# Optimization experiments

Measured on AMD Instinct MI355X. Metric: run time of the kernel, lower is better.

## Reference

```python
import jax, jax.numpy as jnp
import numpy as np

N = 100000
E = 1000000
P = 1000000
HID = 128
ROLE_VOCAB = 8
ROLE_DIM = 16
IDX_VOCAB = 1024
IDX_DIM = 8
FEAT = 14
IN_DIM = FEAT + IDX_DIM + ROLE_DIM  # 38


def setup_inputs() -> dict:
    key = jax.random.key(0)
    ks = jax.random.split(key, 20)
    s = 0.02
    return {
        "block_features": jax.random.normal(ks[0], (N, FEAT), jnp.float32),
        "role_ids": jax.random.randint(ks[1], (N,), 0, ROLE_VOCAB),
        "b2b_src": jax.random.randint(ks[2], (E,), 0, N),
        "b2b_dst": jax.random.randint(ks[3], (E,), 0, N),
        "b2b_w": jax.random.uniform(ks[4], (E,), jnp.float32),
        "p2b_block": jax.random.randint(ks[5], (P,), 0, N),
        "p2b_w": jax.random.uniform(ks[6], (P,), jnp.float32),
        "role_emb": jax.random.normal(ks[7], (ROLE_VOCAB, ROLE_DIM), jnp.float32),
        "idx_emb": jax.random.normal(ks[8], (IDX_VOCAB, IDX_DIM), jnp.float32),
        "W1": jax.random.normal(ks[9], (IN_DIM, HID), jnp.float32) * s,
        "b1": jnp.zeros((HID,), jnp.float32),
        "W2": jax.random.normal(ks[10], (HID, HID), jnp.float32) * s,
        "b2": jnp.zeros((HID,), jnp.float32),
        "M1": jax.random.normal(ks[11], (HID, HID), jnp.float32) * s,
        "mb1": jnp.zeros((HID,), jnp.float32),
        "M2": jax.random.normal(ks[12], (HID, HID), jnp.float32) * s,
        "mb2": jnp.zeros((HID,), jnp.float32),
        "ln_g": jnp.ones((HID,), jnp.float32),
        "ln_b": jnp.zeros((HID,), jnp.float32),
    }


def _layernorm(x, g, b, eps=1e-5):
    mu = jnp.mean(x, axis=-1, keepdims=True)
    var = jnp.mean(jnp.square(x - mu), axis=-1, keepdims=True)
    return (x - mu) * jax.lax.rsqrt(var + eps) * g + b


def reference(block_features, role_ids, b2b_src, b2b_dst, b2b_w, p2b_block, p2b_w,
              role_emb, idx_emb, W1, b1, W2, b2, M1, mb1, M2, mb2, ln_g, ln_b):
    n = block_features.shape[0]
    # embeddings + input MLP
    re = role_emb[role_ids]                                  # [N, 16]
    ie = idx_emb[jnp.arange(n) % IDX_VOCAB]                  # [N, 8]
    x = jnp.concatenate([block_features, re, ie], axis=-1)   # [N, 38]
    h = jax.nn.relu(x @ W1 + b1)
    emb = jax.nn.relu(h @ W2 + b2)                           # [N, HID]
    # b2b: symmetric weighted scatter-add of neighbor embeddings
    agg = jnp.zeros_like(emb)
    agg = agg.at[b2b_src].add(emb[b2b_dst] * b2b_w[:, None])
    agg = agg.at[b2b_dst].add(emb[b2b_src] * b2b_w[:, None])
    # p2b: agg[j] += emb[j] * w  ==  emb * (sum of pin weights per block)
    pw = jnp.zeros((n,), emb.dtype).at[p2b_block].add(p2b_w)
    agg = agg + emb * pw[:, None]
    # message MLP + residual + LayerNorm
    m = jax.nn.relu(agg @ M1 + mb1) @ M2 + mb2
    block_embeddings = _layernorm(emb + m, ln_g, ln_b)
    graph_embedding = jnp.mean(block_embeddings, axis=0)
    return block_embeddings, graph_embedding
```

## Files before the change

kernel.cpp:

```cpp
#include <hip/hip_runtime.h>

#define FEAT 14
#define ROLE_DIM 16
#define IDX_DIM 8
#define IN_DIM 38
#define HID 128
#define IDX_VOCAB 1024
#define BINN 128
#define NBINS_MAX 800
#define TILE_E 2048
#define CAPT 16
#define SCAP 64
#define SORT_CAP 4096

typedef __attribute__((ext_vector_type(8))) short short8;
typedef __attribute__((ext_vector_type(4))) float f32x4;
typedef __attribute__((ext_vector_type(2))) float f32x2;

__device__ __forceinline__ ushort f2bf(float f) {
    uint u = __float_as_uint(f);
    return (ushort)((u + 0x7FFFu + ((u >> 16) & 1u)) >> 16);
}
__device__ __forceinline__ float bf2f(ushort h) {
    return __uint_as_float((uint)h << 16);
}
__device__ __forceinline__ uchar f2fp8(float f) {
    return (uchar)(__builtin_amdgcn_cvt_pk_fp8_f32(f, f, 0, false) & 0xff);
}

__global__ void k_prep(const float* __restrict__ W1, const float* __restrict__ W2,
                       const float* __restrict__ M1, const float* __restrict__ M2,
                       ushort* __restrict__ W1t, ushort* __restrict__ W2t,
                       ushort* __restrict__ M1t, ushort* __restrict__ M2t)
{
    int t = blockIdx.x * 256 + threadIdx.x;
    if (t < 8192) {
        int c = t >> 6, k = t & 63;
        W1t[t] = (k < IN_DIM) ? f2bf(W1[k * HID + c]) : (ushort)0;
    } else if (t < 24576) {
        int u = t - 8192; int c = u >> 7, k = u & 127;
        W2t[u] = f2bf(W2[k * HID + c]);
    } else if (t < 40960) {
        int u = t - 24576; int c = u >> 7, k = u & 127;
        M1t[u] = f2bf(M1[k * HID + c]);
    } else if (t < 57344) {
        int u = t - 40960; int c = u >> 7, k = u & 127;
        M2t[u] = f2bf(M2[k * HID + c]);
    }
}

#define LDSA 32768

__global__ __launch_bounds__(256) void k_embed_mlp(
    const float* __restrict__ feat, const int* __restrict__ role_ids,
    const float* __restrict__ role_emb, const float* __restrict__ idx_emb,
    const ushort* __restrict__ W1t, const float* __restrict__ b1,
    const ushort* __restrict__ W2t, const float* __restrict__ b2,
    ushort* __restrict__ embh, uchar* __restrict__ embf8, int N)
{
    __shared__ char lds[49152];
    const int tid = threadIdx.x;
    const int w = tid >> 6, l = tid & 63;
    const int li = l & 15, hi = l >> 4;
    const int base = blockIdx.x * 64;

    for (int c = 0; c < 4; ++c) {
        int idx = c * 256 + tid;
        int col = idx >> 3, ch = idx & 7;
        uint4 v = *(const uint4*)(W1t + col * 64 + ch * 8);
        *(uint4*)(lds + col * 256 + ((ch * 16) ^ ((col & 7) << 4))) = v;
    }
    {
        int row = tid >> 2, kq = (tid & 3) * 16;
        int gr = base + row; if (gr >= N) gr = N - 1;
        int rid = role_ids[gr];
        float xv[16];
        #pragma unroll
        for (int j = 0; j < 16; ++j) {
            int k = kq + j;
            float v = 0.0f;
            if (k < FEAT)                 v = feat[gr * FEAT + k];
            else if (k < FEAT + ROLE_DIM) v = role_emb[rid * ROLE_DIM + (k - FEAT)];
            else if (k < IN_DIM)          v = idx_emb[(gr & (IDX_VOCAB - 1)) * IDX_DIM + (k - FEAT - ROLE_DIM)];
            xv[j] = v;
        }
        uint p[8];
        #pragma unroll
        for (int j = 0; j < 8; ++j)
            p[j] = (uint)f2bf(xv[2 * j]) | ((uint)f2bf(xv[2 * j + 1]) << 16);
        char* db = lds + LDSA + row * 256;
        int sw = (row & 7) << 4;
        *(uint4*)(db + ((kq * 2) ^ sw))      = make_uint4(p[0], p[1], p[2], p[3]);
        *(uint4*)(db + ((kq * 2 + 16) ^ sw)) = make_uint4(p[4], p[5], p[6], p[7]);
    }
    __syncthreads();

    f32x4 C[8];
    #pragma unroll
    for (int ct = 0; ct < 8; ++ct) C[ct] = (f32x4){0.f, 0.f, 0.f, 0.f};
    {
        const int arow = w * 16 + li;
        const int asw = (arow & 7) << 4;
        #pragma unroll
        for (int ks = 0; ks < 2; ++ks) {
            short8 a = *(short8*)(lds + LDSA + arow * 256 + ((ks * 64 + hi * 16) ^ asw));
            #pragma unroll
            for (int ct = 0; ct < 8; ++ct) {
                int bcol = ct * 16 + li;
                short8 b = *(short8*)(lds + bcol * 256 + ((ks * 64 + hi * 16) ^ ((bcol & 7) << 4)));
                C[ct] = __builtin_amdgcn_mfma_f32_16x16x32_bf16(a, b, C[ct], 0, 0, 0);
            }
        }
    }
    __syncthreads();

    #pragma unroll
    for (int ct = 0; ct < 8; ++ct) {
        int col = ct * 16 + li;
        float bv = b1[col];
        #pragma unroll
        for (int r = 0; r < 4; ++r) {
            int hrow = w * 16 + hi * 4 + r;
            float h = fmaxf(C[ct][r] + bv, 0.0f);
            *(ushort*)(lds + LDSA + hrow * 256 + ((col * 2) ^ ((hrow & 7) << 4))) = f2bf(h);
        }
    }
    for (int c = 0; c < 8; ++c) {
        int idx = c * 256 + tid;
        int col = idx >> 4, ch = idx & 15;
        uint4 v = *(const uint4*)(W2t + col * 128 + ch * 8);
        *(uint4*)(lds + col * 256 + ((ch * 16) ^ ((col & 7) << 4))) = v;
    }
    __syncthreads();

    f32x4 C2[8];
    #pragma unroll
    for (int ct = 0; ct < 8; ++ct) C2[ct] = (f32x4){0.f, 0.f, 0.f, 0.f};
    {
        const int arow = w * 16 + li;
        const int asw = (arow & 7) << 4;
        #pragma unroll
        for (int ks = 0; ks < 4; ++ks) {
            short8 a = *(short8*)(lds + LDSA + arow * 256 + ((ks * 64 + hi * 16) ^ asw));
            #pragma unroll
            for (int ct = 0; ct < 8; ++ct) {
                int bcol = ct * 16 + li;
                short8 b = *(short8*)(lds + bcol * 256 + ((ks * 64 + hi * 16) ^ ((bcol & 7) << 4)));
                C2[ct] = __builtin_amdgcn_mfma_f32_16x16x32_bf16(a, b, C2[ct], 0, 0, 0);
            }
        }
    }

    #pragma unroll
    for (int ct = 0; ct < 8; ++ct) {
        int col = ct * 16 + li;
        float bv = b2[col];
        #pragma unroll
        for (int r = 0; r < 4; ++r) {
            int gr = base + w * 16 + hi * 4 + r;
            if (gr < N) {
                float o = fmaxf(C2[ct][r] + bv, 0.0f);
                embh[(size_t)gr * 128 + col] = f2bf(o);
                embf8[(size_t)gr * 128 + col] = f2fp8(o);
            }
        }
    }
}

__global__ __launch_bounds__(1024) void k_binp(
    const int* __restrict__ src, const int* __restrict__ dst,
    const float* __restrict__ w, uint* __restrict__ staged,
    int* __restrict__ cnt,
    const int* __restrict__ pb, const float* __restrict__ pv,
    float* __restrict__ pw,
    int E, int P, int nbins, int chunk, int chunkP)
{
    __shared__ uint buf[NBINS_MAX * CAPT];
    __shared__ int curT[NBINS_MAX];
    __shared__ int segCur[NBINS_MAX];
    const int tid = threadIdx.x;
    const int blk = blockIdx.x;
    for (int i = tid; i < nbins; i += 1024) { curT[i] = 0; segCur[i] = 0; }
    __syncthreads();

    const int lo = blk * chunk;
    const int hiE = (lo + chunk) < E ? (lo + chunk) : E;
    for (int t0 = lo; t0 < hiE; t0 += TILE_E) {
        int t1 = t0 + TILE_E; if (t1 > hiE) t1 = hiE;
        for (int i = t0 + tid; i < t1; i += 1024) {
            int s = src[i], d = dst[i];
            uint q = (uint)(w[i] * 255.0f + 0.5f);
            int bs = s >> 7;
            uint es = ((uint)(s & 127) << 25) | ((uint)d << 8) | q;
            int ps = atomicAdd(&curT[bs], 1);
            if (ps < CAPT) buf[bs * CAPT + ps] = es;
            else { int gp = segCur[bs] + ps;
                   if (gp < SCAP) staged[((size_t)bs * 256 + blk) * SCAP + gp] = es; }
            int bd = d >> 7;
            uint ed = ((uint)(d & 127) << 25) | ((uint)s << 8) | q;
            int pd = atomicAdd(&curT[bd], 1);
            if (pd < CAPT) buf[bd * CAPT + pd] = ed;
            else { int gp = segCur[bd] + pd;
                   if (gp < SCAP) staged[((size_t)bd * 256 + blk) * SCAP + gp] = ed; }
        }
        __syncthreads();
        for (int b = tid; b < nbins; b += 1024) {
            int tot = curT[b];
            int base = segCur[b];
            int k = tot < CAPT ? tot : CAPT;
            if (base + k > SCAP) { k = SCAP - base; if (k < 0) k = 0; }
            uint* dp = staged + ((size_t)b * 256 + blk) * SCAP + base;
            for (int i = 0; i < k; ++i) dp[i] = buf[b * CAPT + i];
            segCur[b] = base + tot;
            curT[b] = 0;
        }
        __syncthreads();
    }
    for (int i = tid; i < nbins; i += 1024)
        cnt[blk * nbins + i] = segCur[i] < SCAP ? segCur[i] : SCAP;

    int loP = blk * chunkP;
    int hiP = loP + chunkP; if (hiP > P) hiP = P;
    for (int i = loP + tid; i < hiP; i += 1024)
        atomicAdd(&pw[pb[i]], pv[i]);
}

__global__ __launch_bounds__(256) void k_agg(
    const uint* __restrict__ staged, const int* __restrict__ cnt,
    const ushort* __restrict__ embh, const uchar* __restrict__ embf8,
    const float* __restrict__ pw,
    ushort* __restrict__ aggh, int N, int nbins)
{
    __shared__ int hist[BINN];
    __shared__ int startL[BINN];
    __shared__ int curL[BINN];
    __shared__ int sc[BINN];
    __shared__ uint sorted[SORT_CAP];

    const int tid = threadIdx.x;
    const int b = blockIdx.x;
    const int baseNode = b << 7;

    if (tid < BINN) hist[tid] = 0;
    __syncthreads();

    const int c = cnt[tid * nbins + b];
    const uint* sp = staged + ((size_t)b * 256 + tid) * SCAP;
    for (int k = 0; k < c; ++k)
        atomicAdd(&hist[sp[k] >> 25], 1);
    __syncthreads();

    int v = (tid < BINN) ? hist[tid] : 0;
    if (tid < BINN) sc[tid] = v;
    __syncthreads();
    for (int off = 1; off < BINN; off <<= 1) {
        int u = (tid < BINN && tid >= off) ? sc[tid - off] : 0;
        __syncthreads();
        if (tid < BINN) sc[tid] += u;
        __syncthreads();
    }
    if (tid < BINN) {
        startL[tid] = sc[tid] - v;
        curL[tid]   = sc[tid] - v;
    }
    __syncthreads();

    for (int k = 0; k < c; ++k) {
        uint e = sp[k];
        int pos = atomicAdd(&curL[e >> 25], 1);
        if (pos < SORT_CAP) sorted[pos] = e;
    }
    __syncthreads();

    const int g  = tid >> 3;
    const int cg = tid & 7;
    const int c0 = cg * 16;
    for (int h = 0; h < 4; ++h) {
        int nl = h * 32 + g;
        int node = baseNode + nl;
        if (node < N) {
            float acc[16];
            float pwn = pw[node];
            const uint4* r = (const uint4*)(embh + ((size_t)node << 7) + c0);
            uint4 u0 = r[0], u1 = r[1];
            uint uu[8] = {u0.x, u0.y, u0.z, u0.w, u1.x, u1.y, u1.z, u1.w};
            #pragma unroll
            for (int j = 0; j < 8; ++j) {
                acc[2*j]   = __uint_as_float(uu[j] << 16) * pwn;
                acc[2*j+1] = __uint_as_float(uu[j] & 0xffff0000u) * pwn;
            }
            const int st = startL[nl], deg = hist[nl];
            #pragma unroll 4
            for (int i = 0; i < deg; ++i) {
                uint en = sorted[st + i];
                int nb   = (int)((en >> 8) & 0x1FFFFu);
                float wt = (float)(en & 255u) * (1.0f / 255.0f);
                uint4 q = *(const uint4*)(embf8 + ((size_t)nb << 7) + c0);
                uint qq[4] = {q.x, q.y, q.z, q.w};
                #pragma unroll
                for (int j = 0; j < 4; ++j) {
                    f32x2 lo = __builtin_amdgcn_cvt_pk_f32_fp8(qq[j], false);
                    f32x2 hi2 = __builtin_amdgcn_cvt_pk_f32_fp8(qq[j], true);
                    acc[4*j+0] = fmaf(lo.x,  wt, acc[4*j+0]);
                    acc[4*j+1] = fmaf(lo.y,  wt, acc[4*j+1]);
                    acc[4*j+2] = fmaf(hi2.x, wt, acc[4*j+2]);
                    acc[4*j+3] = fmaf(hi2.y, wt, acc[4*j+3]);
                }
            }
            uint p[8];
            #pragma unroll
            for (int j = 0; j < 8; ++j)
                p[j] = (uint)f2bf(acc[2*j]) | ((uint)f2bf(acc[2*j+1]) << 16);
            uint4* ap = (uint4*)(aggh + ((size_t)node << 7) + c0);
            ap[0] = make_uint4(p[0], p[1], p[2], p[3]);
            ap[1] = make_uint4(p[4], p[5], p[6], p[7]);
        }
    }
}

#define LDSS 49152

__global__ __launch_bounds__(256) void k_msg_ln(
    const ushort* __restrict__ aggh, const ushort* __restrict__ embh,
    const ushort* __restrict__ M1t, const ushort* __restrict__ M2t,
    const float* __restrict__ mb1, const float* __restrict__ mb2,
    const float* __restrict__ ln_g, const float* __restrict__ ln_b,
    float* __restrict__ out, float* __restrict__ gsum, int N)
{
    __shared__ char lds[51200];
    const int tid = threadIdx.x;
    const int w = tid >> 6, l = tid & 63;
    const int li = l & 15, hi = l >> 4;
    const int base = blockIdx.x * 64;

    for (int c = 0; c < 8; ++c) {
        int idx = c * 256 + tid;
        int col = idx >> 4, ch = idx & 15;
        uint4 v = *(const uint4*)(M1t + col * 128 + ch * 8);
        *(uint4*)(lds + col * 256 + ((ch * 16) ^ ((col & 7) << 4))) = v;
    }
    for (int c = 0; c < 4; ++c) {
        int idx = c * 256 + tid;
        int row = idx >> 4, ch = idx & 15;
        int gr = base + row; if (gr >= N) gr = N - 1;
        uint4 v = *(const uint4*)(aggh + (size_t)gr * 128 + ch * 8);
        *(uint4*)(lds + LDSA + row * 256 + ((ch * 16) ^ ((row & 7) << 4))) = v;
    }
    __syncthreads();

    f32x4 C[8];
    #pragma unroll
    for (int ct = 0; ct < 8; ++ct) C[ct] = (f32x4){0.f, 0.f, 0.f, 0.f};
    {
        const int arow = w * 16 + li;
        const int asw = (arow & 7) << 4;
        #pragma unroll
        for (int ks = 0; ks < 4; ++ks) {
            short8 a = *(short8*)(lds + LDSA + arow * 256 + ((ks * 64 + hi * 16) ^ asw));
            #pragma unroll
            for (int ct = 0; ct < 8; ++ct) {
                int bcol = ct * 16 + li;
                short8 b = *(short8*)(lds + bcol * 256 + ((ks * 64 + hi * 16) ^ ((bcol & 7) << 4)));
                C[ct] = __builtin_amdgcn_mfma_f32_16x16x32_bf16(a, b, C[ct], 0, 0, 0);
            }
        }
    }
    __syncthreads();

    #pragma unroll
    for (int ct = 0; ct < 8; ++ct) {
        int col = ct * 16 + li;
        float bv = mb1[col];
        #pragma unroll
        for (int r = 0; r < 4; ++r) {
            int hrow = w * 16 + hi * 4 + r;
            float h = fmaxf(C[ct][r] + bv, 0.0f);
            *(ushort*)(lds + LDSA + hrow * 256 + ((col * 2) ^ ((hrow & 7) << 4))) = f2bf(h);
        }
    }
    for (int c = 0; c < 8; ++c) {
        int idx = c * 256 + tid;
        int col = idx >> 4, ch = idx & 15;
        uint4 v = *(const uint4*)(M2t + col * 128 + ch * 8);
        *(uint4*)(lds + col * 256 + ((ch * 16) ^ ((col & 7) << 4))) = v;
    }
    __syncthreads();

    f32x4 C2[8];
    #pragma unroll
    for (int ct = 0; ct < 8; ++ct) C2[ct] = (f32x4){0.f, 0.f, 0.f, 0.f};
    {
        const int arow = w * 16 + li;
        const int asw = (arow & 7) << 4;
        #pragma unroll
        for (int ks = 0; ks < 4; ++ks) {
            short8 a = *(short8*)(lds + LDSA + arow * 256 + ((ks * 64 + hi * 16) ^ asw));
            #pragma unroll
            for (int ct = 0; ct < 8; ++ct) {
                int bcol = ct * 16 + li;
                short8 b = *(short8*)(lds + bcol * 256 + ((ks * 64 + hi * 16) ^ ((bcol & 7) << 4)));
                C2[ct] = __builtin_amdgcn_mfma_f32_16x16x32_bf16(a, b, C2[ct], 0, 0, 0);
            }
        }
    }

    float y[8][4];
    #pragma unroll
    for (int ct = 0; ct < 8; ++ct) {
        int col = ct * 16 + li;
        float bv = mb2[col];
        #pragma unroll
        for (int r = 0; r < 4; ++r) {
            int gr = base + w * 16 + hi * 4 + r;
            int grc = gr < N ? gr : N - 1;
            y[ct][r] = C2[ct][r] + bv + bf2f(embh[(size_t)grc * 128 + col]);
        }
    }
    float rs[4] = {0, 0, 0, 0}, rq[4] = {0, 0, 0, 0};
    #pragma unroll
    for (int ct = 0; ct < 8; ++ct)
        #pragma unroll
        for (int r = 0; r < 4; ++r) { rs[r] += y[ct][r]; rq[r] += y[ct][r] * y[ct][r]; }
    #pragma unroll
    for (int m = 1; m < 16; m <<= 1) {
        #pragma unroll
        for (int r = 0; r < 4; ++r) {
            rs[r] += __shfl_xor(rs[r], m);
            rq[r] += __shfl_xor(rq[r], m);
        }
    }
    float mu[4], rstd[4];
    #pragma unroll
    for (int r = 0; r < 4; ++r) {
        mu[r] = rs[r] * (1.0f / HID);
        float var = rq[r] * (1.0f / HID) - mu[r] * mu[r];
        rstd[r] = rsqrtf(var + 1e-5f);
    }
    float cs[8];
    #pragma unroll
    for (int ct = 0; ct < 8; ++ct) {
        cs[ct] = 0.0f;
        int col = ct * 16 + li;
        float g = ln_g[col], bb = ln_b[col];
        #pragma unroll
        for (int r = 0; r < 4; ++r) {
            int gr = base + w * 16 + hi * 4 + r;
            float o = (y[ct][r] - mu[r]) * rstd[r] * g + bb;
            if (gr < N) {
                out[(size_t)gr * 128 + col] = o;
                cs[ct] += o;
            }
        }
    }
    #pragma unroll
    for (int m = 16; m < 64; m <<= 1) {
        #pragma unroll
        for (int ct = 0; ct < 8; ++ct) cs[ct] += __shfl_xor(cs[ct], m);
    }
    float* wsum = (float*)(lds + LDSS);
    if (hi == 0) {
        #pragma unroll
        for (int ct = 0; ct < 8; ++ct) wsum[w * 128 + ct * 16 + li] = cs[ct];
    }
    __syncthreads();
    if (tid < 128) {
        float s = wsum[tid] + wsum[128 + tid] + wsum[256 + tid] + wsum[384 + tid];
        atomicAdd(&gsum[tid], s);
    }
}

__global__ void k_graph(const float* __restrict__ gsum, float* __restrict__ out,
                        int N)
{
    int j = threadIdx.x;
    out[(size_t)N * HID + j] = gsum[j] * (1.0f / (float)N);
}

extern "C" void kernel_launch(void* const* d_in, const int* in_sizes, int n_in,
                              void* d_out, int out_size, void* d_ws, size_t ws_size,
                              hipStream_t stream)
{
    const float* feat      = (const float*)d_in[0];
    const int*   role_ids  = (const int*)  d_in[1];
    const int*   b2b_src   = (const int*)  d_in[2];
    const int*   b2b_dst   = (const int*)  d_in[3];
    const float* b2b_w     = (const float*)d_in[4];
    const int*   p2b_block = (const int*)  d_in[5];
    const float* p2b_w     = (const float*)d_in[6];
    const float* role_emb  = (const float*)d_in[7];
    const float* idx_emb   = (const float*)d_in[8];
    const float* W1        = (const float*)d_in[9];
    const float* b1        = (const float*)d_in[10];
    const float* W2        = (const float*)d_in[11];
    const float* b2        = (const float*)d_in[12];
    const float* M1        = (const float*)d_in[13];
    const float* mb1       = (const float*)d_in[14];
    const float* M2        = (const float*)d_in[15];
    const float* mb2       = (const float*)d_in[16];
    const float* ln_g      = (const float*)d_in[17];
    const float* ln_b      = (const float*)d_in[18];

    const int N = in_sizes[1];
    const int E = in_sizes[2];
    const int P = in_sizes[5];

    float* out = (float*)d_out;

    const int nbins = (N + BINN - 1) >> 7;
    const int chunk  = (E + 255) / 256;
    const int chunkP = (P + 255) / 256;

    char* ws = (char*)d_ws;
    size_t embhBytes = (size_t)N * HID * sizeof(ushort);
    size_t embf8Bytes= (size_t)N * HID;
    size_t stagBytes = (size_t)nbins * 256 * SCAP * sizeof(uint);
    size_t cntBytes  = (((size_t)256 * nbins * sizeof(int)) + 15) & ~15ull;
    size_t vecBytes  = (size_t)N * sizeof(float);

    ushort* embh    = (ushort*)ws;  ws += embhBytes;
    ushort* aggh    = (ushort*)ws;  ws += embhBytes;
    uchar*  embf8   = (uchar*)ws;   ws += embf8Bytes;
    uint*   staged  = (uint*)ws;    ws += stagBytes;
    int*    cnt     = (int*)ws;     ws += cntBytes;
    float*  pw      = (float*)ws;   ws += vecBytes;
    float*  gsum    = (float*)ws;   ws += 512;
    ushort* W1t     = (ushort*)ws;  ws += 8192  * sizeof(ushort);
    ushort* W2t     = (ushort*)ws;  ws += 16384 * sizeof(ushort);
    ushort* M1t     = (ushort*)ws;  ws += 16384 * sizeof(ushort);
    ushort* M2t     = (ushort*)ws;  ws += 16384 * sizeof(ushort);

    hipMemsetAsync(pw, 0, vecBytes + 512, stream);

    const int nBlocks64 = (N + 63) / 64;

    k_prep<<<224, 256, 0, stream>>>(W1, W2, M1, M2, W1t, W2t, M1t, M2t);

    k_embed_mlp<<<nBlocks64, 256, 0, stream>>>(
        feat, role_ids, role_emb, idx_emb, W1t, b1, W2t, b2, embh, embf8, N);

    k_binp<<<256, 1024, 0, stream>>>(b2b_src, b2b_dst, b2b_w, staged, cnt,
                                     p2b_block, p2b_w, pw, E, P, nbins,
                                     chunk, chunkP);

    k_agg<<<nbins, 256, 0, stream>>>(staged, cnt, embh, embf8, pw, aggh, N, nbins);

    k_msg_ln<<<nBlocks64, 256, 0, stream>>>(
        aggh, embh, M1t, M2t, mb1, mb2, ln_g, ln_b, out, gsum, N);

    k_graph<<<1, HID, 0, stream>>>(gsum, out, N);
}
```

Baseline: 237.3 us.

## Fuse neighbor aggregation with message MLP and LayerNorm in one kernel

Merges the aggregation kernel and the message-MLP/LayerNorm kernel. Each block of 128 nodes now writes its aggregated bf16 rows into swizzled LDS and runs both MFMA matmuls, the residual and LayerNorm directly from there. This removes the global round trip of the aggh intermediate and one kernel launch. In exchange LDS per block grows to about 66KB and the grid is halved to 128-node blocks, which lowers occupancy and parallelism in the matmul phase.

```diff
diff --git a/kernel.cpp b/kernel.cpp
--- a/kernel.cpp
+++ b/kernel.cpp
@@ -225,21 +225,30 @@
         atomicAdd(&pw[pb[i]], pv[i]);
 }
 
-__global__ __launch_bounds__(256) void k_agg(
+#define AREG 32768
+#define WSUM 65536
+
+__global__ __launch_bounds__(256) void k_agg_mlp(
     const uint* __restrict__ staged, const int* __restrict__ cnt,
     const ushort* __restrict__ embh, const uchar* __restrict__ embf8,
     const float* __restrict__ pw,
-    ushort* __restrict__ aggh, int N, int nbins)
+    const ushort* __restrict__ M1t, const ushort* __restrict__ M2t,
+    const float* __restrict__ mb1, const float* __restrict__ mb2,
+    const float* __restrict__ ln_g, const float* __restrict__ ln_b,
+    float* __restrict__ out, float* __restrict__ gsum, int N, int nbins)
 {
-    __shared__ int hist[BINN];
-    __shared__ int startL[BINN];
-    __shared__ int curL[BINN];
-    __shared__ int sc[BINN];
-    __shared__ uint sorted[SORT_CAP];
+    __shared__ char lds[67584];
+    uint* sorted  = (uint*)lds;
+    int*  hist    = (int*)(lds + 16384);
+    int*  startL  = (int*)(lds + 16384 + 512);
+    int*  curL    = (int*)(lds + 16384 + 1024);
+    int*  sc      = (int*)(lds + 16384 + 1536);
 
     const int tid = threadIdx.x;
     const int b = blockIdx.x;
     const int baseNode = b << 7;
+    const int w = tid >> 6, l = tid & 63;
+    const int li = l & 15, hi = l >> 4;
 
     if (tid < BINN) hist[tid] = 0;
     __syncthreads();
@@ -272,192 +281,181 @@
     }
     __syncthreads();
 
-    const int g  = tid >> 3;
-    const int cg = tid & 7;
-    const int c0 = cg * 16;
-    for (int h = 0; h < 4; ++h) {
-        int nl = h * 32 + g;
-        int node = baseNode + nl;
-        if (node < N) {
-            float acc[16];
-            float pwn = pw[node];
-            const uint4* r = (const uint4*)(embh + ((size_t)node << 7) + c0);
-            uint4 u0 = r[0], u1 = r[1];
-            uint uu[8] = {u0.x, u0.y, u0.z, u0.w, u1.x, u1.y, u1.z, u1.w};
-            #pragma unroll
-            for (int j = 0; j < 8; ++j) {
-                acc[2*j]   = __uint_as_float(uu[j] << 16) * pwn;
-                acc[2*j+1] = __uint_as_float(uu[j] & 0xffff0000u) * pwn;
-            }
-            const int st = startL[nl], deg = hist[nl];
-            #pragma unroll 4
-            for (int i = 0; i < deg; ++i) {
-                uint en = sorted[st + i];
-                int nb   = (int)((en >> 8) & 0x1FFFFu);
-                float wt = (float)(en & 255u) * (1.0f / 255.0f);
-                uint4 q = *(const uint4*)(embf8 + ((size_t)nb << 7) + c0);
-                uint qq[4] = {q.x, q.y, q.z, q.w};
+    {
+        const int g  = tid >> 3;
+        const int cg = tid & 7;
+        const int c0 = cg * 16;
+        for (int h = 0; h < 4; ++h) {
+            int nl = h * 32 + g;
+            int node = baseNode + nl;
+            uint p[8];
+            if (node < N) {
+                float acc[16];
+                float pwn = pw[node];
+                const uint4* r = (const uint4*)(embh + ((size_t)node << 7) + c0);
+                uint4 u0 = r[0], u1 = r[1];
+                uint uu[8] = {u0.x, u0.y, u0.z, u0.w, u1.x, u1.y, u1.z, u1.w};
                 #pragma unroll
-                for (int j = 0; j < 4; ++j) {
-                    f32x2 lo = __builtin_amdgcn_cvt_pk_f32_fp8(qq[j], false);
-                    f32x2 hi2 = __builtin_amdgcn_cvt_pk_f32_fp8(qq[j], true);
-                    acc[4*j+0] = fmaf(lo.x,  wt, acc[4*j+0]);
-                    acc[4*j+1] = fmaf(lo.y,  wt, acc[4*j+1]);
-                    acc[4*j+2] = fmaf(hi2.x, wt, acc[4*j+2]);
-                    acc[4*j+3] = fmaf(hi2.y, wt, acc[4*j+3]);
+                for (int j = 0; j < 8; ++j) {
+                    acc[2*j]   = __uint_as_float(uu[j] << 16) * pwn;
+                    acc[2*j+1] = __uint_as_float(uu[j] & 0xffff0000u) * pwn;
                 }
-            }
-            uint p[8];
-            #pragma unroll
-            for (int j = 0; j < 8; ++j)
-                p[j] = (uint)f2bf(acc[2*j]) | ((uint)f2bf(acc[2*j+1]) << 16);
-            uint4* ap = (uint4*)(aggh + ((size_t)node << 7) + c0);
-            ap[0] = make_uint4(p[0], p[1], p[2], p[3]);
-            ap[1] = make_uint4(p[4], p[5], p[6], p[7]);
-        }
-    }
-}
-
-#define LDSS 49152
-
-__global__ __launch_bounds__(256) void k_msg_ln(
-    const ushort* __restrict__ aggh, const ushort* __restrict__ embh,
-    const ushort* __restrict__ M1t, const ushort* __restrict__ M2t,
-    const float* __restrict__ mb1, const float* __restrict__ mb2,
-    const float* __restrict__ ln_g, const float* __restrict__ ln_b,
-    float* __restrict__ out, float* __restrict__ gsum, int N)
-{
-    __shared__ char lds[51200];
-    const int tid = threadIdx.x;
-    const int w = tid >> 6, l = tid & 63;
-    const int li = l & 15, hi = l >> 4;
-    const int base = blockIdx.x * 64;
-
-    for (int c = 0; c < 8; ++c) {
-        int idx = c * 256 + tid;
+                const int st = startL[nl], deg = hist[nl];
+                #pragma unroll 4
+                for (int i = 0; i < deg; ++i) {
+                    uint en = sorted[st + i];
+                    int nb   = (int)((en >> 8) & 0x1FFFFu);
+                    float wt = (float)(en & 255u) * (1.0f / 255.0f);
+                    uint4 q = *(const uint4*)(embf8 + ((size_t)nb << 7) + c0);
+                    uint qq[4] = {q.x, q.y, q.z, q.w};
+                    #pragma unroll
+                    for (int j = 0; j < 4; ++j) {
+                        f32x2 lo = __builtin_amdgcn_cvt_pk_f32_fp8(qq[j], false);
+                        f32x2 hi2 = __builtin_amdgcn_cvt_pk_f32_fp8(qq[j], true);
+                        acc[4*j+0] = fmaf(lo.x,  wt, acc[4*j+0]);
+                        acc[4*j+1] = fmaf(lo.y,  wt, acc[4*j+1]);
+                        acc[4*j+2] = fmaf(hi2.x, wt, acc[4*j+2]);
+                        acc[4*j+3] = fmaf(hi2.y, wt, acc[4*j+3]);
+                    }
+                }
+                #pragma unroll
+                for (int j = 0; j < 8; ++j)
+                    p[j] = (uint)f2bf(acc[2*j]) | ((uint)f2bf(acc[2*j+1]) << 16);
+            } else {
+                #pragma unroll
+                for (int j = 0; j < 8; ++j) p[j] = 0;
+            }
+            char* db = lds + AREG + nl * 256;
+            int sw = (nl & 7) << 4;
+            *(uint4*)(db + ((c0 * 2) ^ sw))      = make_uint4(p[0], p[1], p[2], p[3]);
+            *(uint4*)(db + ((c0 * 2 + 16) ^ sw)) = make_uint4(p[4], p[5], p[6], p[7]);
+        }
+    }
+    __syncthreads();
+
+    for (int cc = 0; cc < 8; ++cc) {
+        int idx = cc * 256 + tid;
         int col = idx >> 4, ch = idx & 15;
-        uint4 v = *(const uint4*)(M1t + col * 128 + ch * 8);
-        *(uint4*)(lds + col * 256 + ((ch * 16) ^ ((col & 7) << 4))) = v;
-    }
-    for (int c = 0; c < 4; ++c) {
-        int idx = c * 256 + tid;
-        int row = idx >> 4, ch = idx & 15;
-        int gr = base + row; if (gr >= N) gr = N - 1;
-        uint4 v = *(const uint4*)(aggh + (size_t)gr * 128 + ch * 8);
-        *(uint4*)(lds + LDSA + row * 256 + ((ch * 16) ^ ((row & 7) << 4))) = v;
-    }
-    __syncthreads();
-
-    f32x4 C[8];
-    #pragma unroll
-    for (int ct = 0; ct < 8; ++ct) C[ct] = (f32x4){0.f, 0.f, 0.f, 0.f};
-    {
-        const int arow = w * 16 + li;
+        uint4 vv = *(const uint4*)(M1t + col * 128 + ch * 8);
+        *(uint4*)(lds + col * 256 + ((ch * 16) ^ ((col & 7) << 4))) = vv;
+    }
+    __syncthreads();
+
+    #pragma unroll
+    for (int h2 = 0; h2 < 2; ++h2) {
+        f32x4 C1[8];
+        #pragma unroll
+        for (int ct = 0; ct < 8; ++ct) C1[ct] = (f32x4){0.f, 0.f, 0.f, 0.f};
+        const int arow = h2 * 64 + w * 16 + li;
         const int asw = (arow & 7) << 4;
         #pragma unroll
         for (int ks = 0; ks < 4; ++ks) {
-            short8 a = *(short8*)(lds + LDSA + arow * 256 + ((ks * 64 + hi * 16) ^ asw));
+            short8 a = *(short8*)(lds + AREG + arow * 256 + ((ks * 64 + hi * 16) ^ asw));
             #pragma unroll
             for (int ct = 0; ct < 8; ++ct) {
                 int bcol = ct * 16 + li;
-                short8 b = *(short8*)(lds + bcol * 256 + ((ks * 64 + hi * 16) ^ ((bcol & 7) << 4)));
-                C[ct] = __builtin_amdgcn_mfma_f32_16x16x32_bf16(a, b, C[ct], 0, 0, 0);
-            }
-        }
-    }
-    __syncthreads();
-
-    #pragma unroll
-    for (int ct = 0; ct < 8; ++ct) {
-        int col = ct * 16 + li;
-        float bv = mb1[col];
-        #pragma unroll
-        for (int r = 0; r < 4; ++r) {
-            int hrow = w * 16 + hi * 4 + r;
-            float h = fmaxf(C[ct][r] + bv, 0.0f);
-            *(ushort*)(lds + LDSA + hrow * 256 + ((col * 2) ^ ((hrow & 7) << 4))) = f2bf(h);
-        }
-    }
-    for (int c = 0; c < 8; ++c) {
-        int idx = c * 256 + tid;
+                short8 bb = *(short8*)(lds + bcol * 256 + ((ks * 64 + hi * 16) ^ ((bcol & 7) << 4)));
+                C1[ct] = __builtin_amdgcn_mfma_f32_16x16x32_bf16(a, bb, C1[ct], 0, 0, 0);
+            }
+        }
+        #pragma unroll
+        for (int ct = 0; ct < 8; ++ct) {
+            int col = ct * 16 + li;
+            float bv = mb1[col];
+            #pragma unroll
+            for (int r = 0; r < 4; ++r) {
+                int hrow = h2 * 64 + w * 16 + hi * 4 + r;
+                float h = fmaxf(C1[ct][r] + bv, 0.0f);
+                *(ushort*)(lds + AREG + hrow * 256 + ((col * 2) ^ ((hrow & 7) << 4))) = f2bf(h);
+            }
+        }
+    }
+    __syncthreads();
+
+    for (int cc = 0; cc < 8; ++cc) {
+        int idx = cc * 256 + tid;
         int col = idx >> 4, ch = idx & 15;
-        uint4 v = *(const uint4*)(M2t + col * 128 + ch * 8);
-        *(uint4*)(lds + col * 256 + ((ch * 16) ^ ((col & 7) << 4))) = v;
-    }
-    __syncthreads();
-
-    f32x4 C2[8];
-    #pragma unroll
-    for (int ct = 0; ct < 8; ++ct) C2[ct] = (f32x4){0.f, 0.f, 0.f, 0.f};
-    {
-        const int arow = w * 16 + li;
+        uint4 vv = *(const uint4*)(M2t + col * 128 + ch * 8);
+        *(uint4*)(lds + col * 256 + ((ch * 16) ^ ((col & 7) << 4))) = vv;
+    }
+    __syncthreads();
+
+    float cs[8];
+    #pragma unroll
+    for (int ct = 0; ct < 8; ++ct) cs[ct] = 0.0f;
+
+    #pragma unroll
+    for (int h2 = 0; h2 < 2; ++h2) {
+        f32x4 C2[8];
+        #pragma unroll
+        for (int ct = 0; ct < 8; ++ct) C2[ct] = (f32x4){0.f, 0.f, 0.f, 0.f};
+        const int arow = h2 * 64 + w * 16 + li;
         const int asw = (arow & 7) << 4;
         #pragma unroll
         for (int ks = 0; ks < 4; ++ks) {
-            short8 a = *(short8*)(lds + LDSA + arow * 256 + ((ks * 64 + hi * 16) ^ asw));
+            short8 a = *(short8*)(lds + AREG + arow * 256 + ((ks * 64 + hi * 16) ^ asw));
             #pragma unroll
             for (int ct = 0; ct < 8; ++ct) {
                 int bcol = ct * 16 + li;
-                short8 b = *(short8*)(lds + bcol * 256 + ((ks * 64 + hi * 16) ^ ((bcol & 7) << 4)));
-                C2[ct] = __builtin_amdgcn_mfma_f32_16x16x32_bf16(a, b, C2[ct], 0, 0, 0);
-            }
-        }
-    }
-
-    float y[8][4];
-    #pragma unroll
-    for (int ct = 0; ct < 8; ++ct) {
-        int col = ct * 16 + li;
-        float bv = mb2[col];
+                short8 bb = *(short8*)(lds + bcol * 256 + ((ks * 64 + hi * 16) ^ ((bcol & 7) << 4)));
+                C2[ct] = __builtin_amdgcn_mfma_f32_16x16x32_bf16(a, bb, C2[ct], 0, 0, 0);
+            }
+        }
+
+        float y[8][4];
+        #pragma unroll
+        for (int ct = 0; ct < 8; ++ct) {
+            int col = ct * 16 + li;
+            float bv = mb2[col];
+            #pragma unroll
+            for (int r = 0; r < 4; ++r) {
+                int gr = baseNode + h2 * 64 + w * 16 + hi * 4 + r;
+                int grc = gr < N ? gr : N - 1;
+                y[ct][r] = C2[ct][r] + bv + bf2f(embh[(size_t)grc * 128 + col]);
+            }
+        }
+        float rs[4] = {0, 0, 0, 0}, rq[4] = {0, 0, 0, 0};
+        #pragma unroll
+        for (int ct = 0; ct < 8; ++ct)
+            #pragma unroll
+            for (int r = 0; r < 4; ++r) { rs[r] += y[ct][r]; rq[r] += y[ct][r] * y[ct][r]; }
+        #pragma unroll
+        for (int m = 1; m < 16; m <<= 1) {
+            #pragma unroll
+            for (int r = 0; r < 4; ++r) {
+                rs[r] += __shfl_xor(rs[r], m);
+                rq[r] += __shfl_xor(rq[r], m);
+            }
+        }
+        float mu[4], rstd[4];
         #pragma unroll
         for (int r = 0; r < 4; ++r) {
-            int gr = base + w * 16 + hi * 4 + r;
-            int grc = gr < N ? gr : N - 1;
-            y[ct][r] = C2[ct][r] + bv + bf2f(embh[(size_t)grc * 128 + col]);
-        }
-    }
-    float rs[4] = {0, 0, 0, 0}, rq[4] = {0, 0, 0, 0};
-    #pragma unroll
-    for (int ct = 0; ct < 8; ++ct)
-        #pragma unroll
-        for (int r = 0; r < 4; ++r) { rs[r] += y[ct][r]; rq[r] += y[ct][r] * y[ct][r]; }
-    #pragma unroll
-    for (int m = 1; m < 16; m <<= 1) {
-        #pragma unroll
-        for (int r = 0; r < 4; ++r) {
-            rs[r] += __shfl_xor(rs[r], m);
-            rq[r] += __shfl_xor(rq[r], m);
-        }
-    }
-    float mu[4], rstd[4];
-    #pragma unroll
-    for (int r = 0; r < 4; ++r) {
-        mu[r] = rs[r] * (1.0f / HID);
-        float var = rq[r] * (1.0f / HID) - mu[r] * mu[r];
-        rstd[r] = rsqrtf(var + 1e-5f);
-    }
-    float cs[8];
-    #pragma unroll
-    for (int ct = 0; ct < 8; ++ct) {
-        cs[ct] = 0.0f;
-        int col = ct * 16 + li;
-        float g = ln_g[col], bb = ln_b[col];
-        #pragma unroll
-        for (int r = 0; r < 4; ++r) {
-            int gr = base + w * 16 + hi * 4 + r;
-            float o = (y[ct][r] - mu[r]) * rstd[r] * g + bb;
-            if (gr < N) {
-                out[(size_t)gr * 128 + col] = o;
-                cs[ct] += o;
-            }
-        }
-    }
+            mu[r] = rs[r] * (1.0f / HID);
+            float var = rq[r] * (1.0f / HID) - mu[r] * mu[r];
+            rstd[r] = rsqrtf(var + 1e-5f);
+        }
+        #pragma unroll
+        for (int ct = 0; ct < 8; ++ct) {
+            int col = ct * 16 + li;
+            float g = ln_g[col], bb2 = ln_b[col];
+            #pragma unroll
+            for (int r = 0; r < 4; ++r) {
+                int gr = baseNode + h2 * 64 + w * 16 + hi * 4 + r;
+                float o = (y[ct][r] - mu[r]) * rstd[r] * g + bb2;
+                if (gr < N) {
+                    out[(size_t)gr * 128 + col] = o;
+                    cs[ct] += o;
+                }
+            }
+        }
+    }
+
     #pragma unroll
     for (int m = 16; m < 64; m <<= 1) {
         #pragma unroll
         for (int ct = 0; ct < 8; ++ct) cs[ct] += __shfl_xor(cs[ct], m);
     }
-    float* wsum = (float*)(lds + LDSS);
+    float* wsum = (float*)(lds + WSUM);
     if (hi == 0) {
         #pragma unroll
         for (int ct = 0; ct < 8; ++ct) wsum[w * 128 + ct * 16 + li] = cs[ct];
@@ -518,7 +516,6 @@
     size_t vecBytes  = (size_t)N * sizeof(float);
 
     ushort* embh    = (ushort*)ws;  ws += embhBytes;
-    ushort* aggh    = (ushort*)ws;  ws += embhBytes;
     uchar*  embf8   = (uchar*)ws;   ws += embf8Bytes;
     uint*   staged  = (uint*)ws;    ws += stagBytes;
     int*    cnt     = (int*)ws;     ws += cntBytes;
@@ -542,10 +539,9 @@
                                      p2b_block, p2b_w, pw, E, P, nbins,
                                      chunk, chunkP);
 
-    k_agg<<<nbins, 256, 0, stream>>>(staged, cnt, embh, embf8, pw, aggh, N, nbins);
-
-    k_msg_ln<<<nBlocks64, 256, 0, stream>>>(
-        aggh, embh, M1t, M2t, mb1, mb2, ln_g, ln_b, out, gsum, N);
+    k_agg_mlp<<<nbins, 256, 0, stream>>>(
+        staged, cnt, embh, embf8, pw, M1t, M2t, mb1, mb2, ln_g, ln_b,
+        out, gsum, N, nbins);
 
     k_graph<<<1, HID, 0, stream>>>(gsum, out, N);
 }
```

After: 232.7 us. Within noise of the previous version (-1.9%).
